# Performance work log

Measured on AMD Instinct MI355X. Metric: run time of the kernel, lower is better.

## Reference

```python
import jax, jax.numpy as jnp
import numpy as np

B, C, Q, E, H = 8, 1024, 128, 512, 1024


def setup_inputs() -> dict:
    key = jax.random.key(0)
    ks = jax.random.split(key, 8)
    return {
        "context": jax.random.normal(ks[0], (B, C, E), jnp.float32),
        "question": jax.random.normal(ks[1], (B, Q, E), jnp.float32),
        "context_mask": jnp.ones((B, C), jnp.float32),
        "w_question": jax.random.normal(ks[2], (E,), jnp.float32),
        "w_context": jax.random.normal(ks[3], (E,), jnp.float32),
        "w_multiple": jax.random.normal(ks[4], (E,), jnp.float32),
        "W1": jax.random.normal(ks[5], (4 * E, H), jnp.float32) * 0.02,
        "b1": jnp.zeros((H,), jnp.float32),
        "W2": jax.random.normal(ks[6], (H, 4 * E), jnp.float32) * 0.02,
        "b2": jnp.zeros((4 * E,), jnp.float32),
    }


def reference(context, question, context_mask, w_question, w_context, w_multiple, W1, b1, W2, b2):
    # Dropout is identity at eval time.
    # Trilinear similarity: s[b,c,q] = q.w_q + ctx.w_c + sum_e q_e*ctx_e*w_m_e
    q_w = question @ w_question                                  # (B,Q)
    c_w = context @ w_context                                    # (B,C)
    mult = jnp.einsum("bqe,bce->bcq", question * w_multiple, context)  # avoids (B,C,Q,E)
    sim = q_w[:, None, :] + c_w[:, :, None] + mult               # (B,C,Q)

    # Context2Query: softmax over question dim (dim=2)
    c2q = jnp.einsum("bcq,bqe->bce", jax.nn.softmax(sim, axis=2), question)
    # Query2Context: max over question dim, softmax over context dim (dim=1)
    q2c = jnp.einsum("bc,bce->be", jax.nn.softmax(jnp.max(sim, axis=2), axis=1), context)  # (B,E)

    attended = jnp.concatenate(
        [context, c2q, context * c2q, context * q2c[:, None, :]], axis=2
    )  # (B,C,4E)

    # MaskedLinear: linear then zero out masked context positions
    m = context_mask[:, :, None]
    h = (attended @ W1 + b1) * m
    out = jax.nn.relu((h @ W2 + b2) * m)
    return out
```

## Files before the change

kernel.cpp:

```cpp
#include <hip/hip_runtime.h>

typedef __bf16 bf16;
typedef __bf16 bf16x2 __attribute__((ext_vector_type(2)));
typedef __bf16 bf16x4 __attribute__((ext_vector_type(4)));
typedef __bf16 bf16x8 __attribute__((ext_vector_type(8)));
typedef float f32x4 __attribute__((ext_vector_type(4)));

#define AS1 __attribute__((address_space(1)))
#define AS3 __attribute__((address_space(3)))

__device__ __forceinline__ void async_copy16(const void* g, void* l) {
  __builtin_amdgcn_global_load_lds((const AS1 void*)g, (AS3 void*)l, 16, 0, 0);
}

#define BB 8
#define CC 1024
#define QQ 128
#define EE 512
#define HH 1024
#define FOURE 2048

__global__ __launch_bounds__(256) void prep_kernel(
    const float* __restrict__ W1, const float* __restrict__ W2,
    const float* __restrict__ qst, const float* __restrict__ wmul,
    const float* __restrict__ wqv, bf16* __restrict__ W1T,
    bf16* __restrict__ W2T, bf16* __restrict__ qT,
    bf16* __restrict__ qmh, bf16* __restrict__ qml, float* __restrict__ qw) {
  __shared__ float tile[32][33];
  __shared__ float r4[4];
  int bx = blockIdx.x;
  int t = threadIdx.x;
  if (bx >= 4608) {
    int i = bx - 4608;
    int half = t >> 7, tr = t & 127;
    int rowg = i * 2 + half;
    const float* qrow = qst + (size_t)rowg * EE;
    float4 qv = *(const float4*)&qrow[tr * 4];
    float4 wm4 = *(const float4*)&wmul[tr * 4];
    float4 wq4 = *(const float4*)&wqv[tr * 4];
    float m[4] = {qv.x * wm4.x, qv.y * wm4.y, qv.z * wm4.z, qv.w * wm4.w};
    bf16x4 h, l;
#pragma unroll
    for (int k = 0; k < 4; ++k) {
      bf16 hh = (bf16)m[k];
      h[k] = hh; l[k] = (bf16)(m[k] - (float)hh);
    }
    *(bf16x4*)&qmh[(size_t)rowg * EE + tr * 4] = h;
    *(bf16x4*)&qml[(size_t)rowg * EE + tr * 4] = l;
    float s = qv.x * wq4.x + qv.y * wq4.y + qv.z * wq4.z + qv.w * wq4.w;
#pragma unroll
    for (int off = 32; off; off >>= 1) s += __shfl_xor(s, off);
    if ((t & 63) == 0) r4[t >> 6] = s;
    __syncthreads();
    if (tr == 0) qw[rowg] = r4[half * 2] + r4[half * 2 + 1];
    return;
  }
  const float* src;
  bf16* dst;
  int R, C, idx;
  if (bx < 2048) {
    src = W1; dst = W1T; R = 2048; C = 1024; idx = bx;
  } else if (bx < 4096) {
    src = W2; dst = W2T; R = 1024; C = 2048; idx = bx - 2048;
  } else {
    int i = bx - 4096;
    int b = i >> 6; idx = i & 63;
    src = qst + (size_t)b * QQ * EE; dst = qT + (size_t)b * EE * QQ;
    R = 128; C = 512;
  }
  int ctiles = C >> 5;
  int by = idx / ctiles, cx = idx % ctiles;
  int tx = t & 31, ty = t >> 5;
#pragma unroll
  for (int rr = 0; rr < 4; ++rr)
    tile[ty + rr * 8][tx] = src[(size_t)(by * 32 + ty + rr * 8) * C + cx * 32 + tx];
  __syncthreads();
#pragma unroll
  for (int rr = 0; rr < 4; ++rr)
    dst[(size_t)(cx * 32 + ty + rr * 8) * R + by * 32 + tx] = (bf16)tile[tx][ty + rr * 8];
}

__global__ __launch_bounds__(256) void fused_att_kernel(
    const float* __restrict__ ctx, const bf16* __restrict__ qmh,
    const bf16* __restrict__ qml, const bf16* __restrict__ qT,
    const float* __restrict__ wc, const float* __restrict__ qw,
    float* __restrict__ smax, bf16* __restrict__ att) {
  int b = blockIdx.y;
  int m0 = blockIdx.x * 16;
  __shared__ __align__(16) char U[26880];
  bf16* Ah = (bf16*)(U);
  bf16* Al = (bf16*)(U + 1024);
  bf16* Bh = (bf16*)(U + 2048);
  bf16* Bl = (bf16*)(U + 10240);
  float(*sim_s)[132] = (float(*)[132])(U + 18432);
  bf16* c2q_lds = (bf16*)(U);
  __shared__ float wc_s[EE];
  __shared__ float qw_s[QQ];
  __shared__ float cw_s[16];
  __shared__ bf16 P_lds[16][136];
  int t = threadIdx.x;
  for (int i = t; i < EE; i += 256) wc_s[i] = wc[i];
  if (t < QQ) qw_s[t] = qw[b * QQ + t];
  __syncthreads();
  int wv = t >> 6, ln = t & 63;
  int rl = ln & 15, kq = ln >> 4;
  f32x4 acc[2] = {};
  const float* Ag = ctx + ((size_t)b * CC + m0) * EE;
  const bf16* Bhg = qmh + (size_t)b * QQ * EE;
  const bf16* Blg = qml + (size_t)b * QQ * EE;
  int arow = t >> 4, ae = (t & 15) * 2;
  float cwp = 0.f;
  for (int k0 = 0; k0 < EE; k0 += 32) {
    {
      float2 v = *(const float2*)(Ag + (size_t)arow * EE + k0 + ae);
      cwp += v.x * wc_s[k0 + ae] + v.y * wc_s[k0 + ae + 1];
      bf16 h0 = (bf16)v.x, h1 = (bf16)v.y;
      bf16x2 h, l;
      h[0] = h0; h[1] = h1;
      l[0] = (bf16)(v.x - (float)h0);
      l[1] = (bf16)(v.y - (float)h1);
      int sl = ((ae >> 3) ^ ((arow >> 1) & 3)) * 8 + (ae & 7);
      *(bf16x2*)&Ah[arow * 32 + sl] = h;
      *(bf16x2*)&Al[arow * 32 + sl] = l;
    }
#pragma unroll
    for (int r = 0; r < 2; ++r) {
      int fb = (r * 4 + wv) * 1024 + ln * 16;
      int row = fb >> 6;
      int cq = ((fb >> 4) & 3) ^ ((row >> 1) & 3);
      async_copy16(Bhg + (size_t)row * EE + k0 + cq * 8, (char*)Bh + fb);
      async_copy16(Blg + (size_t)row * EE + k0 + cq * 8, (char*)Bl + fb);
    }
    __syncthreads();
    bf16x8 ah, al, bh[2], bl[2];
    {
      int sl = (kq ^ ((rl >> 1) & 3)) * 8;
      ah = *(const bf16x8*)&Ah[rl * 32 + sl];
      al = *(const bf16x8*)&Al[rl * 32 + sl];
    }
#pragma unroll
    for (int j = 0; j < 2; ++j) {
      int r = wv * 32 + j * 16 + rl;
      int sl = (kq ^ ((r >> 1) & 3)) * 8;
      bh[j] = *(const bf16x8*)&Bh[r * 32 + sl];
      bl[j] = *(const bf16x8*)&Bl[r * 32 + sl];
    }
#pragma unroll
    for (int j = 0; j < 2; ++j) {
      acc[j] = __builtin_amdgcn_mfma_f32_16x16x32_bf16(ah, bh[j], acc[j], 0, 0, 0);
      acc[j] = __builtin_amdgcn_mfma_f32_16x16x32_bf16(ah, bl[j], acc[j], 0, 0, 0);
      acc[j] = __builtin_amdgcn_mfma_f32_16x16x32_bf16(al, bh[j], acc[j], 0, 0, 0);
    }
    __syncthreads();
  }
  {
    float s = cwp;
    s += __shfl_xor(s, 1); s += __shfl_xor(s, 2);
    s += __shfl_xor(s, 4); s += __shfl_xor(s, 8);
    if ((t & 15) == 0) cw_s[arow] = s;
  }
#pragma unroll
  for (int j = 0; j < 2; ++j) {
    int col = wv * 32 + j * 16 + rl;
    float qv = qw_s[col];
    int rbase = kq * 4;
#pragma unroll
    for (int r = 0; r < 4; ++r) sim_s[rbase + r][col] = acc[j][r] + qv;
  }
  __syncthreads();
  {
    int row = t >> 4, cb = t & 15;
    float v[8];
    float mx = -3.4e38f;
#pragma unroll
    for (int k = 0; k < 8; ++k) {
      v[k] = sim_s[row][cb + 16 * k];
      mx = fmaxf(mx, v[k]);
    }
    mx = fmaxf(mx, __shfl_xor(mx, 1));
    mx = fmaxf(mx, __shfl_xor(mx, 2));
    mx = fmaxf(mx, __shfl_xor(mx, 4));
    mx = fmaxf(mx, __shfl_xor(mx, 8));
    float sm = 0.f;
#pragma unroll
    for (int k = 0; k < 8; ++k) { v[k] = __expf(v[k] - mx); sm += v[k]; }
    sm += __shfl_xor(sm, 1);
    sm += __shfl_xor(sm, 2);
    sm += __shfl_xor(sm, 4);
    sm += __shfl_xor(sm, 8);
    float inv = 1.0f / sm;
#pragma unroll
    for (int k = 0; k < 8; ++k) P_lds[row][cb + 16 * k] = (bf16)(v[k] * inv);
    if (cb == 0) smax[b * CC + m0 + row] = mx + cw_s[row];
  }
  __syncthreads();
  f32x4 acc2[8] = {};
  const bf16* qTb = qT + (size_t)b * EE * QQ;
#pragma unroll
  for (int kk = 0; kk < 4; ++kk) {
    bf16x8 af2;
    {
      bf16x4 lo = *(const bf16x4*)&P_lds[rl][kk * 32 + kq * 8];
      bf16x4 hi = *(const bf16x4*)&P_lds[rl][kk * 32 + kq * 8 + 4];
      af2[0] = lo[0]; af2[1] = lo[1]; af2[2] = lo[2]; af2[3] = lo[3];
      af2[4] = hi[0]; af2[5] = hi[1]; af2[6] = hi[2]; af2[7] = hi[3];
    }
#pragma unroll
    for (int j = 0; j < 8; ++j) {
      int n = wv * 128 + j * 16 + rl;
      bf16x8 bfr = *(const bf16x8*)&qTb[(size_t)n * QQ + kk * 32 + kq * 8];
      acc2[j] = __builtin_amdgcn_mfma_f32_16x16x32_bf16(af2, bfr, acc2[j], 0, 0, 0);
    }
  }
#pragma unroll
  for (int j = 0; j < 8; ++j) {
    int col = wv * 128 + j * 16 + rl;
    int rbase = kq * 4;
#pragma unroll
    for (int r = 0; r < 4; ++r)
      c2q_lds[(size_t)(rbase + r) * 520 + col] = (bf16)acc2[j][r];
  }
  __syncthreads();
  {
    int row = t >> 4, tc = t & 15;
    const float* crow = ctx + ((size_t)(b * CC + m0 + row)) * EE;
    bf16* arow_p = att + ((size_t)(b * CC + m0 + row)) * FOURE;
#pragma unroll
    for (int cc = 0; cc < 4; ++cc) {
      int col = cc * 128 + tc * 8;
      bf16x8 q8 = *(const bf16x8*)&c2q_lds[(size_t)row * 520 + col];
      float4 v0 = *(const float4*)&crow[col];
      float4 v1 = *(const float4*)&crow[col + 4];
      float cv[8] = {v0.x, v0.y, v0.z, v0.w, v1.x, v1.y, v1.z, v1.w};
      bf16x8 o0, o2;
#pragma unroll
      for (int k = 0; k < 8; ++k) {
        o0[k] = (bf16)cv[k];
        o2[k] = (bf16)(cv[k] * (float)q8[k]);
      }
      *(bf16x8*)&arow_p[col] = o0;
      *(bf16x8*)&arow_p[EE + col] = q8;
      *(bf16x8*)&arow_p[2 * EE + col] = o2;
    }
  }
}

__global__ __launch_bounds__(256) void q2c_kernel(
    const float* __restrict__ ctx, const float* __restrict__ smax,
    float* __restrict__ q2c) {
  int b = blockIdx.x >> 5, ch = blockIdx.x & 31;
  int t = threadIdx.x;
  __shared__ float red[256];
  __shared__ float w_s[32];
  float v[4];
  float mx = -3.4e38f;
#pragma unroll
  for (int i = 0; i < 4; ++i) {
    v[i] = smax[b * CC + i * 256 + t];
    mx = fmaxf(mx, v[i]);
  }
  red[t] = mx;
  __syncthreads();
  for (int s = 128; s > 0; s >>= 1) {
    if (t < s) red[t] = fmaxf(red[t], red[t + s]);
    __syncthreads();
  }
  mx = red[0];
  __syncthreads();
  float sm = 0.f;
#pragma unroll
  for (int i = 0; i < 4; ++i) sm += __expf(v[i] - mx);
  red[t] = sm;
  __syncthreads();
  for (int s = 128; s > 0; s >>= 1) {
    if (t < s) red[t] += red[t + s];
    __syncthreads();
  }
  float inv = 1.0f / red[0];
  if (t < 32) w_s[t] = __expf(smax[b * CC + ch * 32 + t] - mx) * inv;
  __syncthreads();
  int e = t * 2;
  const float* cb = ctx + ((size_t)b * CC + ch * 32) * EE;
  float a0 = 0.f, a1 = 0.f;
#pragma unroll 8
  for (int r = 0; r < 32; ++r) {
    float2 vv = *(const float2*)&cb[(size_t)r * EE + e];
    float w = w_s[r];
    a0 += w * vv.x;
    a1 += w * vv.y;
  }
  atomicAdd(&q2c[b * EE + e], a0);
  atomicAdd(&q2c[b * EE + e + 1], a1);
}

__global__ __launch_bounds__(256) void att3_kernel(
    const float* __restrict__ ctx, const float* __restrict__ q2c,
    bf16* __restrict__ att) {
  int idx = blockIdx.x * 256 + threadIdx.x;
  int row = idx >> 6;
  int e = (idx & 63) * 8;
  int b = row >> 10;
  float4 v0 = *(const float4*)&ctx[(size_t)row * EE + e];
  float4 v1 = *(const float4*)&ctx[(size_t)row * EE + e + 4];
  float4 g0 = *(const float4*)&q2c[b * EE + e];
  float4 g1 = *(const float4*)&q2c[b * EE + e + 4];
  bf16x8 o;
  o[0] = (bf16)(v0.x * g0.x); o[1] = (bf16)(v0.y * g0.y);
  o[2] = (bf16)(v0.z * g0.z); o[3] = (bf16)(v0.w * g0.w);
  o[4] = (bf16)(v1.x * g1.x); o[5] = (bf16)(v1.y * g1.y);
  o[6] = (bf16)(v1.z * g1.z); o[7] = (bf16)(v1.w * g1.w);
  *(bf16x8*)&att[(size_t)row * FOURE + 3 * EE + e] = o;
}

template <int MT, int OUT_BF16, int RELU, int HAS_BIAS, int HAS_MASK>
__global__ __launch_bounds__(256) void gemm_bt_kernel(
    const bf16* __restrict__ A, const bf16* __restrict__ Bt,
    const float* __restrict__ bias, const float* __restrict__ mask,
    void* __restrict__ Cout, int M, int N, int K, long sA, long sB, long sC) {
  int b = blockIdx.y;
  A += (size_t)b * sA;
  Bt += (size_t)b * sB;
  int ntiles = N >> 7;
  int tiles_per_g = 8 * ntiles;
  int g = blockIdx.x / tiles_per_g, sub = blockIdx.x % tiles_per_g;
  int mt = g * 8 + (sub & 7), ntb = sub >> 3;
  int m0 = mt * MT, n0 = ntb << 7;
  __shared__ bf16 As[MT * 64];
  __shared__ bf16 Bs[128 * 64];
  int t = threadIdx.x, wv = t >> 6, ln = t & 63;
  int wm = wv >> 1, wn = wv & 1;
  constexpr int MI = MT / 32;
  f32x4 acc[MI][4] = {};
  for (int k0 = 0; k0 < K; k0 += 64) {
#pragma unroll
    for (int r = 0; r < MT / 32; ++r) {
      int fb = (r * 4 + wv) * 1024 + ln * 16;
      int row = fb >> 7;
      int q = ((fb >> 4) & 7) ^ (row & 7);
      async_copy16(A + (size_t)(m0 + row) * K + k0 + q * 8,
                   (char*)As + fb);
    }
#pragma unroll
    for (int r = 0; r < 4; ++r) {
      int fb = (r * 4 + wv) * 1024 + ln * 16;
      int row = fb >> 7;
      int q = ((fb >> 4) & 7) ^ (row & 7);
      async_copy16(Bt + (size_t)(n0 + row) * K + k0 + q * 8,
                   (char*)Bs + fb);
    }
    __syncthreads();
    int rl = ln & 15, kq = ln >> 4;
#pragma unroll
    for (int ks = 0; ks < 2; ++ks) {
      int c = ks * 4 + kq;
      bf16x8 af[MI], bfr[4];
#pragma unroll
      for (int i = 0; i < MI; ++i) {
        int row = wm * (MT / 2) + i * 16 + rl;
        af[i] = *(const bf16x8*)&As[row * 64 + ((c ^ (row & 7)) * 8)];
      }
#pragma unroll
      for (int j = 0; j < 4; ++j) {
        int row = wn * 64 + j * 16 + rl;
        bfr[j] = *(const bf16x8*)&Bs[row * 64 + ((c ^ (row & 7)) * 8)];
      }
#pragma unroll
      for (int i = 0; i < MI; ++i)
#pragma unroll
        for (int j = 0; j < 4; ++j)
          acc[i][j] = __builtin_amdgcn_mfma_f32_16x16x32_bf16(af[i], bfr[j], acc[i][j], 0, 0, 0);
    }
    __syncthreads();
  }
  size_t outbase = (size_t)b * sC;
#pragma unroll
  for (int j = 0; j < 4; ++j) {
    int col = n0 + wn * 64 + j * 16 + (ln & 15);
    float bv = HAS_BIAS ? bias[col] : 0.f;
#pragma unroll
    for (int i = 0; i < MI; ++i) {
      int rbase = m0 + wm * (MT / 2) + i * 16 + ((ln >> 4) << 2);
#pragma unroll
      for (int r = 0; r < 4; ++r) {
        int row = rbase + r;
        float v = acc[i][j][r] + bv;
        if (HAS_MASK) v *= mask[row];
        if (RELU) v = fmaxf(v, 0.f);
        if (OUT_BF16)
          ((bf16*)Cout)[outbase + (size_t)row * N + col] = (bf16)v;
        else
          ((float*)Cout)[outbase + (size_t)row * N + col] = v;
      }
    }
  }
}

extern "C" void kernel_launch(void* const* d_in, const int* in_sizes, int n_in,
                              void* d_out, int out_size, void* d_ws, size_t ws_size,
                              hipStream_t stream) {
  const float* ctx = (const float*)d_in[0];
  const float* qst = (const float*)d_in[1];
  const float* mask = (const float*)d_in[2];
  const float* wqv = (const float*)d_in[3];
  const float* wcv = (const float*)d_in[4];
  const float* wmul = (const float*)d_in[5];
  const float* W1 = (const float*)d_in[6];
  const float* b1 = (const float*)d_in[7];
  const float* W2 = (const float*)d_in[8];
  const float* b2 = (const float*)d_in[9];
  float* out = (float*)d_out;
  char* ws = (char*)d_ws;

  bf16* att = (bf16*)(ws);
  bf16* hbuf = (bf16*)(ws + 33554432);
  bf16* W1T = (bf16*)(ws + 50331648);
  bf16* W2T = (bf16*)(ws + 54525952);
  bf16* qT = (bf16*)(ws + 58720256);
  bf16* qmh = (bf16*)(ws + 59768832);
  bf16* qml = (bf16*)(ws + 60817408);
  float* smax = (float*)(ws + 61865984);
  float* q2c = (float*)(ws + 61898752);
  float* qw = (float*)(ws + 61915136);

  prep_kernel<<<5120, 256, 0, stream>>>(W1, W2, qst, wmul, wqv,
                                        W1T, W2T, qT, qmh, qml, qw);
  fused_att_kernel<<<dim3(64, BB), 256, 0, stream>>>(ctx, qmh, qml, qT, wcv,
                                                     qw, smax, att);
  hipMemsetAsync(q2c, 0, BB * EE * sizeof(float), stream);
  q2c_kernel<<<256, 256, 0, stream>>>(ctx, smax, q2c);
  att3_kernel<<<2048, 256, 0, stream>>>(ctx, q2c, att);
  gemm_bt_kernel<128, 1, 0, 1, 1><<<dim3(512, 1), 256, 0, stream>>>(
      att, W1T, b1, mask, hbuf, 8192, 1024, 2048, 0, 0, 0);
  gemm_bt_kernel<128, 0, 1, 1, 1><<<dim3(1024, 1), 256, 0, stream>>>(
      hbuf, W2T, b2, mask, out, 8192, 2048, 1024, 0, 0, 0);
}
```

Measured before the change: 230.9 us.

## Triple-buffer async LDS loads in GEMMs with 128x256 tiles and 512 threads

Replaces the single-buffered GEMM with a three-stage ring of LDS buffers. Global-to-LDS async copies for tile k+2 are issued while tile k is being computed, using vmcnt waits and raw barriers instead of two __syncthreads per iteration. The block tile grows to 128x256 with 8 waves, and an XCD-aware block swizzle is added. This is meant to hide global load latency and raise MFMA utilisation. In exchange it uses about 144KB of LDS per block, which limits occupancy to one block per CU despite the launch bound of 2, and halves the grid size.

```diff
diff --git a/kernel.cpp b/kernel.cpp
--- a/kernel.cpp
+++ b/kernel.cpp
@@ -312,84 +312,107 @@
   *(bf16x8*)&att[(size_t)row * FOURE + 3 * EE + e] = o;
 }
 
-template <int MT, int OUT_BF16, int RELU, int HAS_BIAS, int HAS_MASK>
-__global__ __launch_bounds__(256) void gemm_bt_kernel(
+template <int OUT_BF16, int RELU>
+__global__ __launch_bounds__(512, 2) void gemm_bt_db_kernel(
     const bf16* __restrict__ A, const bf16* __restrict__ Bt,
     const float* __restrict__ bias, const float* __restrict__ mask,
-    void* __restrict__ Cout, int M, int N, int K, long sA, long sB, long sC) {
-  int b = blockIdx.y;
-  A += (size_t)b * sA;
-  Bt += (size_t)b * sB;
-  int ntiles = N >> 7;
-  int tiles_per_g = 8 * ntiles;
-  int g = blockIdx.x / tiles_per_g, sub = blockIdx.x % tiles_per_g;
-  int mt = g * 8 + (sub & 7), ntb = sub >> 3;
-  int m0 = mt * MT, n0 = ntb << 7;
-  __shared__ bf16 As[MT * 64];
-  __shared__ bf16 Bs[128 * 64];
+    void* __restrict__ Cout, int M, int N, int K) {
+  __shared__ bf16 As[3][128 * 64];
+  __shared__ bf16 Bs[3][256 * 64];
+  int ntn = N >> 8;
+  int nblk = (M >> 7) * ntn;
+  int cpx = nblk >> 3;
+  int bid = blockIdx.x;
+  int swz = (bid & 7) * cpx + (bid >> 3);
+  int mt = swz / ntn, ntb = swz - mt * ntn;
+  int m0 = mt << 7, n0 = ntb << 8;
   int t = threadIdx.x, wv = t >> 6, ln = t & 63;
-  int wm = wv >> 1, wn = wv & 1;
-  constexpr int MI = MT / 32;
-  f32x4 acc[MI][4] = {};
-  for (int k0 = 0; k0 < K; k0 += 64) {
-#pragma unroll
-    for (int r = 0; r < MT / 32; ++r) {
-      int fb = (r * 4 + wv) * 1024 + ln * 16;
+  int wm = wv >> 2, wn = wv & 3;
+  int rl = ln & 15, kq = ln >> 4;
+  int NT = K >> 6;
+
+  auto stage = [&](int buf, int kt) {
+    int k0 = kt << 6;
+#pragma unroll
+    for (int r = 0; r < 2; ++r) {
+      int fb = r * 8192 + t * 16;
       int row = fb >> 7;
       int q = ((fb >> 4) & 7) ^ (row & 7);
       async_copy16(A + (size_t)(m0 + row) * K + k0 + q * 8,
-                   (char*)As + fb);
+                   (char*)As[buf] + fb);
     }
 #pragma unroll
     for (int r = 0; r < 4; ++r) {
-      int fb = (r * 4 + wv) * 1024 + ln * 16;
+      int fb = r * 8192 + t * 16;
       int row = fb >> 7;
       int q = ((fb >> 4) & 7) ^ (row & 7);
       async_copy16(Bt + (size_t)(n0 + row) * K + k0 + q * 8,
-                   (char*)Bs + fb);
-    }
-    __syncthreads();
-    int rl = ln & 15, kq = ln >> 4;
+                   (char*)Bs[buf] + fb);
+    }
+  };
+
+  stage(0, 0);
+  stage(1, 1);
+  asm volatile("s_waitcnt vmcnt(6)" ::: "memory");
+  __builtin_amdgcn_s_barrier();
+  asm volatile("" ::: "memory");
+
+  f32x4 acc[4][4] = {};
+  int cur = 0, nx2 = 2;
+  for (int tt = 0; tt < NT; ++tt) {
+    if (tt + 2 < NT) stage(nx2, tt + 2);
+    const bf16* Ab = As[cur];
+    const bf16* Bb = Bs[cur];
 #pragma unroll
     for (int ks = 0; ks < 2; ++ks) {
       int c = ks * 4 + kq;
-      bf16x8 af[MI], bfr[4];
-#pragma unroll
-      for (int i = 0; i < MI; ++i) {
-        int row = wm * (MT / 2) + i * 16 + rl;
-        af[i] = *(const bf16x8*)&As[row * 64 + ((c ^ (row & 7)) * 8)];
+      bf16x8 af[4], bfr[4];
+#pragma unroll
+      for (int i = 0; i < 4; ++i) {
+        int row = wm * 64 + i * 16 + rl;
+        af[i] = *(const bf16x8*)&Ab[row * 64 + ((c ^ (row & 7)) * 8)];
       }
 #pragma unroll
       for (int j = 0; j < 4; ++j) {
         int row = wn * 64 + j * 16 + rl;
-        bfr[j] = *(const bf16x8*)&Bs[row * 64 + ((c ^ (row & 7)) * 8)];
+        bfr[j] = *(const bf16x8*)&Bb[row * 64 + ((c ^ (row & 7)) * 8)];
       }
 #pragma unroll
-      for (int i = 0; i < MI; ++i)
+      for (int i = 0; i < 4; ++i)
 #pragma unroll
         for (int j = 0; j < 4; ++j)
-          acc[i][j] = __builtin_amdgcn_mfma_f32_16x16x32_bf16(af[i], bfr[j], acc[i][j], 0, 0, 0);
-    }
-    __syncthreads();
-  }
-  size_t outbase = (size_t)b * sC;
+          acc[i][j] = __builtin_amdgcn_mfma_f32_16x16x32_bf16(
+              af[i], bfr[j], acc[i][j], 0, 0, 0);
+    }
+    if (tt + 1 < NT) {
+      if (tt + 2 < NT)
+        asm volatile("s_waitcnt vmcnt(6)" ::: "memory");
+      else
+        asm volatile("s_waitcnt vmcnt(0)" ::: "memory");
+      __builtin_amdgcn_s_barrier();
+      asm volatile("" ::: "memory");
+    }
+    cur = cur == 2 ? 0 : cur + 1;
+    nx2 = nx2 == 2 ? 0 : nx2 + 1;
+  }
+
 #pragma unroll
   for (int j = 0; j < 4; ++j) {
-    int col = n0 + wn * 64 + j * 16 + (ln & 15);
-    float bv = HAS_BIAS ? bias[col] : 0.f;
-#pragma unroll
-    for (int i = 0; i < MI; ++i) {
-      int rbase = m0 + wm * (MT / 2) + i * 16 + ((ln >> 4) << 2);
+    int col = n0 + wn * 64 + j * 16 + rl;
+    float bv = bias[col];
+#pragma unroll
+    for (int i = 0; i < 4; ++i) {
+      int rbase = m0 + wm * 64 + i * 16 + (kq << 2);
 #pragma unroll
       for (int r = 0; r < 4; ++r) {
         int row = rbase + r;
         float v = acc[i][j][r] + bv;
-        if (HAS_MASK) v *= mask[row];
+        v *= mask[row];
         if (RELU) v = fmaxf(v, 0.f);
         if (OUT_BF16)
-          ((bf16*)Cout)[outbase + (size_t)row * N + col] = (bf16)v;
+          ((bf16*)Cout)[(size_t)row * N + col] = (bf16)v;
         else
-          ((float*)Cout)[outbase + (size_t)row * N + col] = v;
+          ((float*)Cout)[(size_t)row * N + col] = v;
       }
     }
   }
@@ -429,8 +452,8 @@
   hipMemsetAsync(q2c, 0, BB * EE * sizeof(float), stream);
   q2c_kernel<<<256, 256, 0, stream>>>(ctx, smax, q2c);
   att3_kernel<<<2048, 256, 0, stream>>>(ctx, q2c, att);
-  gemm_bt_kernel<128, 1, 0, 1, 1><<<dim3(512, 1), 256, 0, stream>>>(
-      att, W1T, b1, mask, hbuf, 8192, 1024, 2048, 0, 0, 0);
-  gemm_bt_kernel<128, 0, 1, 1, 1><<<dim3(1024, 1), 256, 0, stream>>>(
-      hbuf, W2T, b2, mask, out, 8192, 2048, 1024, 0, 0, 0);
-}
+  gemm_bt_db_kernel<1, 0><<<256, 512, 0, stream>>>(
+      att, W1T, b1, mask, hbuf, 8192, 1024, 2048);
+  gemm_bt_db_kernel<0, 1><<<512, 512, 0, stream>>>(
+      hbuf, W2T, b2, mask, out, 8192, 2048, 1024);
+}
```

After: 238.5 us. 1.03x slower.
